# Kernel optimization log

Hardware: AMD Instinct MI355X
Metric: run time of the kernel (lower is better)

Reference implementation:

```python
import jax, jax.numpy as jnp
import numpy as np

NU, NP, H = 100000, 200000, 128
EV, EL = 500000, 150000


def _sage(x_src, x_dst, src, dst, Wl, bl, Wr, n_dst):
    # PyG SAGEConv: lin_l(mean_j x_j) + lin_r(x_i); lin_l has bias, lin_r does not.
    msg = x_src[src]                                             # [E, H] gather
    agg = jax.ops.segment_sum(msg, dst, num_segments=n_dst)      # [n_dst, H]
    cnt = jax.ops.segment_sum(jnp.ones((src.shape[0],), x_src.dtype), dst,
                              num_segments=n_dst)                # [n_dst]
    mean = agg / jnp.maximum(cnt, 1.0)[:, None]
    return mean @ Wl.T + bl + x_dst @ Wr.T


def _hetero_layer(xu, xp, Wl, bl, Wr, ev_s, ev_d, el_s, el_d):
    # relation order: 0 viewed(u->p), 1 rev_viewed(p->u), 2 liked(u->p), 3 rev_liked(p->u)
    post = (_sage(xu, xp, ev_s, ev_d, Wl[0], bl[0], Wr[0], NP)
            + _sage(xu, xp, el_s, el_d, Wl[2], bl[2], Wr[2], NP))
    user = (_sage(xp, xu, ev_d, ev_s, Wl[1], bl[1], Wr[1], NU)
            + _sage(xp, xu, el_d, el_s, Wl[3], bl[3], Wr[3], NU))
    return user, post


def setup_inputs() -> dict:
    key = jax.random.key(0)
    ks = jax.random.split(key, 9)
    s = 1.0 / np.sqrt(H)
    return {
        "emb_user": jax.random.normal(ks[0], (NU, H), jnp.float32),
        "emb_post": jax.random.normal(ks[1], (NP, H), jnp.float32),
        "W_l": jax.random.normal(ks[2], (2, 4, H, H), jnp.float32) * s,
        "b_l": jnp.zeros((2, 4, H), jnp.float32),
        "W_r": jax.random.normal(ks[3], (2, 4, H, H), jnp.float32) * s,
        "viewed_src": jax.random.randint(ks[4], (EV,), 0, NU, jnp.int32),
        "viewed_dst": jax.random.randint(ks[5], (EV,), 0, NP, jnp.int32),
        "liked_src": jax.random.randint(ks[6], (EL,), 0, NU, jnp.int32),
        "liked_dst": jax.random.randint(ks[7], (EL,), 0, NP, jnp.int32),
    }


def reference(emb_user, emb_post, W_l, b_l, W_r,
              viewed_src, viewed_dst, liked_src, liked_dst):
    xu, xp = _hetero_layer(emb_user, emb_post, W_l[0], b_l[0], W_r[0],
                           viewed_src, viewed_dst, liked_src, liked_dst)
    xu, xp = jax.nn.relu(xu), jax.nn.relu(xp)
    xu, xp = _hetero_layer(xu, xp, W_l[1], b_l[1], W_r[1],
                           viewed_src, viewed_dst, liked_src, liked_dst)
    return xu, xp
```

## Files before the change

kernel.cpp:

```cpp
#include <hip/hip_runtime.h>
#include <hip/hip_bf16.h>

#define H 128
#define IDX_CAP 2048

using bf16x8  = __attribute__((ext_vector_type(8))) short;
using floatx4 = __attribute__((ext_vector_type(4))) float;

static __device__ __forceinline__ short f2bf(float f) {
  union { float f; unsigned u; } v; v.f = f;
  unsigned r = v.u + 0x7fffu + ((v.u >> 16) & 1u);
  return (short)(r >> 16);
}
static __device__ __forceinline__ float bf2f(short s) {
  union { unsigned u; float f; } v; v.u = ((unsigned)(unsigned short)s) << 16;
  return v.f;
}

__global__ void count_edges(const int* __restrict__ src, const int* __restrict__ dst,
                            int E, int* __restrict__ cnt_s, int* __restrict__ cnt_d) {
  int e = blockIdx.x * blockDim.x + threadIdx.x;
  if (e >= E) return;
  atomicAdd(&cnt_s[src[e]], 1);
  atomicAdd(&cnt_d[dst[e]], 1);
}

__global__ __launch_bounds__(256) void scan_k1(const int* __restrict__ cnt, int* __restrict__ off,
                                               int* __restrict__ bsums, int4 starts, int4 lens) {
  int a = blockIdx.y;
  int start = ((const int*)&starts)[a];
  int len   = ((const int*)&lens)[a];
  int chunk = blockIdx.x * 1024;
  if (chunk >= len) return;
  const int* in = cnt + start;
  int* out = off + start;
  int tid = threadIdx.x;
  int base = chunk + tid * 4;
  int v[4];
#pragma unroll
  for (int j = 0; j < 4; ++j) v[j] = (base + j < len) ? in[base + j] : 0;
  int s = v[0] + v[1] + v[2] + v[3];
  __shared__ int lds[256];
  lds[tid] = s; __syncthreads();
  for (int o = 1; o < 256; o <<= 1) {
    int t = (tid >= o) ? lds[tid - o] : 0;
    __syncthreads();
    lds[tid] += t;
    __syncthreads();
  }
  int run = lds[tid] - s;
#pragma unroll
  for (int j = 0; j < 4; ++j) { if (base + j < len) out[base + j] = run; run += v[j]; }
  if (tid == 255) bsums[a * 256 + blockIdx.x] = lds[255];
}

__global__ __launch_bounds__(256) void scan_k2(int* __restrict__ bsums, int4 lens) {
  int a = blockIdx.x;
  int len = ((const int*)&lens)[a];
  int nb = (len + 1023) >> 10;
  int tid = threadIdx.x;
  int s = (tid < nb) ? bsums[a * 256 + tid] : 0;
  __shared__ int lds[256];
  lds[tid] = s; __syncthreads();
  for (int o = 1; o < 256; o <<= 1) {
    int t = (tid >= o) ? lds[tid - o] : 0;
    __syncthreads();
    lds[tid] += t;
    __syncthreads();
  }
  bsums[a * 256 + tid] = lds[tid] - s;
}

__global__ __launch_bounds__(256) void scan_k3(int* __restrict__ off, const int* __restrict__ bsums,
                                               int4 starts, int4 lens) {
  int a = blockIdx.y;
  int start = ((const int*)&starts)[a];
  int len   = ((const int*)&lens)[a];
  int chunk = blockIdx.x * 1024;
  if (chunk >= len) return;
  int add = bsums[a * 256 + blockIdx.x];
  int* out = off + start;
  int base = chunk + threadIdx.x * 4;
#pragma unroll
  for (int j = 0; j < 4; ++j) if (base + j < len) out[base + j] += add;
}

__global__ void fill_csr(const int* __restrict__ src, const int* __restrict__ dst, int E,
                         const int* __restrict__ off_d, int* __restrict__ cur_d, int* __restrict__ sort_d,
                         const int* __restrict__ off_s, int* __restrict__ cur_s, int* __restrict__ sort_s) {
  int e = blockIdx.x * blockDim.x + threadIdx.x;
  if (e >= E) return;
  int s = src[e], d = dst[e];
  sort_d[off_d[d] + atomicAdd(&cur_d[d], 1)] = s;
  sort_s[off_s[s] + atomicAdd(&cur_s[s], 1)] = d;
}

__global__ void cvt_bf16(const float* __restrict__ in, short* __restrict__ out, int n) {
  int idx = (blockIdx.x * blockDim.x + threadIdx.x) * 4;
  if (idx >= n) return;
  float4 v = *(const float4*)(in + idx);
  short4 o = { f2bf(v.x), f2bf(v.y), f2bf(v.z), f2bf(v.w) };
  *(short4*)(out + idx) = o;
}

static __device__ __forceinline__ int wswz(int e) {
  int n = e >> 7, k = e & 127;
  int jt = n >> 4, r = n & 15;
  int kk = k >> 5, q = (k >> 3) & 3, j = k & 7;
  return (((jt * 4 + kk) * 64 + q * 16 + r) << 3) + j;
}
__global__ void prep_weights(const float* __restrict__ W_l, const float* __restrict__ b_l,
                             const float* __restrict__ W_r,
                             short* __restrict__ Wbf, float* __restrict__ bc) {
  int i = blockIdx.x * blockDim.x + threadIdx.x;
  if (i >= 4 * 16384) return;
  int s = i >> 14, e = i & 16383;
  int l = s >> 1, t = s & 1;
  int rA = t ? 1 : 0, rB = t ? 3 : 2;
  const float* WA = W_l + ((size_t)(l * 4 + rA) << 14);
  const float* WB = W_l + ((size_t)(l * 4 + rB) << 14);
  const float* RA = W_r + ((size_t)(l * 4 + rA) << 14);
  const float* RB = W_r + ((size_t)(l * 4 + rB) << 14);
  short* o = Wbf + (size_t)s * 3 * 16384;
  int d = wswz(e);
  o[d]             = f2bf(WA[e]);
  o[16384 + d]     = f2bf(WB[e]);
  o[2 * 16384 + d] = f2bf(RA[e] + RB[e]);
  if (e < H) bc[s * H + e] = b_l[(l * 4 + rA) * H + e] + b_l[(l * 4 + rB) * H + e];
}

__global__ __launch_bounds__(512, 2) void fused_layer(
    const short* __restrict__ xgA, const short* __restrict__ xbA,
    const int* __restrict__ sVA, const int* __restrict__ oVA, const int* __restrict__ cVA,
    const int* __restrict__ sLA, const int* __restrict__ oLA, const int* __restrict__ cLA,
    const short* __restrict__ WAp, const float* __restrict__ biasA,
    float* __restrict__ o32A, short* __restrict__ o16A, int NA, int nbA,
    const short* __restrict__ xgB, const short* __restrict__ xbB,
    const int* __restrict__ sVB, const int* __restrict__ oVB, const int* __restrict__ cVB,
    const int* __restrict__ sLB, const int* __restrict__ oLB, const int* __restrict__ cLB,
    const short* __restrict__ WBp, const float* __restrict__ biasB,
    float* __restrict__ o32B, short* __restrict__ o16B, int NB, int relu) {
  extern __shared__ short smem[];
  short* Wlds = smem;
  int* idxLds = (int*)(smem + 3 * 16384);

  int b = blockIdx.x;
  const short *xg, *xb, *W; const int *sV, *oV, *cV, *sL, *oL, *cL;
  const float* bias; float* out32; short* out16; int N, nbPart, bLoc;
  if (b < nbA) {
    xg = xgA; xb = xbA; sV = sVA; oV = oVA; cV = cVA; sL = sLA; oL = oLA; cL = cLA;
    W = WAp; bias = biasA; out32 = o32A; out16 = o16A; N = NA; nbPart = nbA; bLoc = b;
  } else {
    xg = xgB; xb = xbB; sV = sVB; oV = oVB; cV = cVB; sL = sLB; oL = oLB; cL = cLB;
    W = WBp; bias = biasB; out32 = o32B; out16 = o16B; N = NB;
    nbPart = gridDim.x - nbA; bLoc = b - nbA;
  }

  int tid = threadIdx.x;
#pragma unroll
  for (int it = 0; it < 12; ++it) {
    int c = it * 512 + tid;
    *(bf16x8*)(Wlds + (size_t)c * 8) = *(const bf16x8*)(W + (size_t)c * 8);
  }
  __syncthreads();

  int wave = tid >> 6, lane = tid & 63;
  int r = lane & 15, quad = lane >> 4;
  int* myIdx = idxLds + wave * IDX_CAP;

  float bias_r[8];
#pragma unroll
  for (int jt = 0; jt < 8; ++jt) bias_r[jt] = bias[jt * 16 + r];

  int nrgTot = (N + 31) >> 5;
  int wStride = nbPart * 8;
  int wBase = bLoc * 8 + wave;

  floatx4 acc[2][8];

  for (int rg = wBase; rg < nrgTot; rg += wStride) {
    int rowb = rg << 5;

    bf16x8 afX[2][4];
#pragma unroll
    for (int t = 0; t < 2; ++t) {
      int row = rowb + t * 16 + r;
      row = row < N ? row : N - 1;
      const short* Xr = xb + (size_t)row * H + quad * 8;
#pragma unroll
      for (int kk = 0; kk < 4; ++kk) afX[t][kk] = *(const bf16x8*)(Xr + kk * 32);
    }

    int rbL = rowb + 31; rbL = rbL < N ? rbL : N - 1;
    int OV0 = oV[rowb];
    int lenV = oV[rbL] + cV[rbL] - OV0;
    int OL0 = oL[rowb];
    int lenL = oL[rbL] + cL[rbL] - OL0;
    int capV = lenV < IDX_CAP ? lenV : IDX_CAP;
    int rem = IDX_CAP - capV;
    int capL = lenL < rem ? lenL : rem;
    for (int k = lane; k < capV; k += 64) myIdx[k] = sV[OV0 + k];
    for (int k = lane; k < capL; k += 64) myIdx[capV + k] = sL[OL0 + k];

#pragma unroll
    for (int t = 0; t < 2; ++t)
#pragma unroll
      for (int j = 0; j < 8; ++j) acc[t][j] = floatx4{0.f, 0.f, 0.f, 0.f};

    bf16x8 afm[2][4];

    auto gatherRel = [&](const int* __restrict__ offA, const int* __restrict__ cntA,
                         const int* __restrict__ sG, int O0, int base, int cap) {
#pragma unroll
      for (int t = 0; t < 2; ++t) {
        int row = rowb + t * 16 + r;
        int node = row < N ? row : N - 1;
        int o = offA[node], n = cntA[node];
        int lo = o - O0;
        float ag[4][8];
#pragma unroll
        for (int kk = 0; kk < 4; ++kk)
#pragma unroll
          for (int j = 0; j < 8; ++j) ag[kk][j] = 0.f;

        auto gidx = [&](int i) -> int {
          int li = lo + i;
          return (li < cap) ? myIdx[base + li] : sG[o + i];
        };

        bf16x8 pA[4], pB[4];
        if (n > 0) {
          const short* xr = xg + (size_t)gidx(0) * H + quad * 8;
#pragma unroll
          for (int kk = 0; kk < 4; ++kk) pA[kk] = *(const bf16x8*)(xr + kk * 32);
        }
        if (n > 1) {
          const short* xr = xg + (size_t)gidx(1) * H + quad * 8;
#pragma unroll
          for (int kk = 0; kk < 4; ++kk) pB[kk] = *(const bf16x8*)(xr + kk * 32);
        }
        for (int i = 0; i < n; i += 2) {
          bf16x8 nA[4], nB[4];
          if (i + 2 < n) {
            const short* xr = xg + (size_t)gidx(i + 2) * H + quad * 8;
#pragma unroll
            for (int kk = 0; kk < 4; ++kk) nA[kk] = *(const bf16x8*)(xr + kk * 32);
          }
          if (i + 3 < n) {
            const short* xr = xg + (size_t)gidx(i + 3) * H + quad * 8;
#pragma unroll
            for (int kk = 0; kk < 4; ++kk) nB[kk] = *(const bf16x8*)(xr + kk * 32);
          }
#pragma unroll
          for (int kk = 0; kk < 4; ++kk)
#pragma unroll
            for (int j = 0; j < 8; ++j) ag[kk][j] += bf2f(pA[kk][j]);
          if (i + 1 < n) {
#pragma unroll
            for (int kk = 0; kk < 4; ++kk)
#pragma unroll
              for (int j = 0; j < 8; ++j) ag[kk][j] += bf2f(pB[kk][j]);
          }
#pragma unroll
          for (int kk = 0; kk < 4; ++kk) { pA[kk] = nA[kk]; pB[kk] = nB[kk]; }
        }
        float rin = 1.0f / fmaxf((float)n, 1.0f);
#pragma unroll
        for (int kk = 0; kk < 4; ++kk) {
          bf16x8 w;
#pragma unroll
          for (int j = 0; j < 8; ++j) w[j] = f2bf(ag[kk][j] * rin);
          afm[t][kk] = w;
        }
      }
    };

    auto mfmaMat = [&](int m, bf16x8 (&af)[2][4]) {
      const short* Wm = Wlds + m * 16384;
#pragma unroll
      for (int kk = 0; kk < 4; ++kk) {
#pragma unroll
        for (int jt = 0; jt < 8; ++jt) {
          bf16x8 bfR = *(const bf16x8*)(Wm + (size_t)((jt * 4 + kk) * 64 + lane) * 8);
          acc[0][jt] = __builtin_amdgcn_mfma_f32_16x16x32_bf16(af[0][kk], bfR, acc[0][jt], 0, 0, 0);
          acc[1][jt] = __builtin_amdgcn_mfma_f32_16x16x32_bf16(af[1][kk], bfR, acc[1][jt], 0, 0, 0);
        }
      }
    };

    gatherRel(oV, cV, sV, OV0, 0, capV);
    mfmaMat(0, afm);
    gatherRel(oL, cL, sL, OL0, capV, capL);
    mfmaMat(1, afm);
    mfmaMat(2, afX);

#pragma unroll
    for (int t = 0; t < 2; ++t) {
#pragma unroll
      for (int jt = 0; jt < 8; ++jt) {
        int ocol = jt * 16 + r;
        float bv = bias_r[jt];
#pragma unroll
        for (int g = 0; g < 4; ++g) {
          int orow = rowb + t * 16 + quad * 4 + g;
          if (orow < N) {
            float v = acc[t][jt][g] + bv;
            if (relu) v = fmaxf(v, 0.f);
            if (out32) out32[(size_t)orow * H + ocol] = v;
            else       out16[(size_t)orow * H + ocol] = f2bf(v);
          }
        }
      }
    }
  }
}

extern "C" void kernel_launch(void* const* d_in, const int* in_sizes, int n_in,
                              void* d_out, int out_size, void* d_ws, size_t ws_size,
                              hipStream_t stream) {
  const float* emb_user = (const float*)d_in[0];
  const float* emb_post = (const float*)d_in[1];
  const float* W_l = (const float*)d_in[2];
  const float* b_l = (const float*)d_in[3];
  const float* W_r = (const float*)d_in[4];
  const int* ev_s = (const int*)d_in[5];
  const int* ev_d = (const int*)d_in[6];
  const int* el_s = (const int*)d_in[7];
  const int* el_d = (const int*)d_in[8];

  const int NU = in_sizes[0] / H;
  const int NP = in_sizes[1] / H;
  const int EV = in_sizes[5];
  const int EL = in_sizes[7];
  const int T = 2 * NP + 2 * NU;
  const size_t NUH = (size_t)NU * H, NPH = (size_t)NP * H;

  char* p = (char*)d_ws;
  auto alloc = [&](size_t bytes) -> void* {
    void* q = (void*)p; p += (bytes + 255) & ~(size_t)255; return q;
  };
  int*   cnt   = (int*)alloc((size_t)T * 4);
  int*   cur   = (int*)alloc((size_t)T * 4);
  int*   off   = (int*)alloc((size_t)T * 4);
  int*   bsums = (int*)alloc(4 * 256 * 4);
  int*   sV_p  = (int*)alloc((size_t)EV * 4);
  int*   sV_u  = (int*)alloc((size_t)EV * 4);
  int*   sL_p  = (int*)alloc((size_t)EL * 4);
  int*   sL_u  = (int*)alloc((size_t)EL * 4);
  short* Wbf   = (short*)alloc((size_t)4 * 3 * 16384 * 2);
  float* bc    = (float*)alloc(4 * H * 4);
  short* xbf_u  = (short*)alloc(NUH * 2);
  short* xbf_p  = (short*)alloc(NPH * 2);
  short* xbf1_u = (short*)alloc(NUH * 2);
  short* xbf1_p = (short*)alloc(NPH * 2);

  float* out_u_final = (float*)d_out;
  float* out_p_final = (float*)d_out + NUH;

  const int oV_p = 0, oL_p = NP, oV_u = 2 * NP, oL_u = 2 * NP + NU;

  hipMemsetAsync(cnt, 0, (size_t)T * 4, stream);
  hipMemsetAsync(cur, 0, (size_t)T * 4, stream);
  count_edges<<<(EV + 255) / 256, 256, 0, stream>>>(ev_s, ev_d, EV, cnt + oV_u, cnt + oV_p);
  count_edges<<<(EL + 255) / 256, 256, 0, stream>>>(el_s, el_d, EL, cnt + oL_u, cnt + oL_p);

  int4 starts = { oV_p, oL_p, oV_u, oL_u };
  int4 lens   = { NP, NP, NU, NU };
  int maxb = ((NP > NU ? NP : NU) + 1023) / 1024;
  dim3 gscan(maxb, 4, 1);
  scan_k1<<<gscan, 256, 0, stream>>>(cnt, off, bsums, starts, lens);
  scan_k2<<<4, 256, 0, stream>>>(bsums, lens);
  scan_k3<<<gscan, 256, 0, stream>>>(off, bsums, starts, lens);

  fill_csr<<<(EV + 255) / 256, 256, 0, stream>>>(ev_s, ev_d, EV,
                                                 off + oV_p, cur + oV_p, sV_p,
                                                 off + oV_u, cur + oV_u, sV_u);
  fill_csr<<<(EL + 255) / 256, 256, 0, stream>>>(el_s, el_d, EL,
                                                 off + oL_p, cur + oL_p, sL_p,
                                                 off + oL_u, cur + oL_u, sL_u);

  cvt_bf16<<<((int)(NUH / 4) + 255) / 256, 256, 0, stream>>>(emb_user, xbf_u, (int)NUH);
  cvt_bf16<<<((int)(NPH / 4) + 255) / 256, 256, 0, stream>>>(emb_post, xbf_p, (int)NPH);
  prep_weights<<<(4 * 16384 + 255) / 256, 256, 0, stream>>>(W_l, b_l, W_r, Wbf, bc);

  hipFuncSetAttribute((const void*)fused_layer, hipFuncAttributeMaxDynamicSharedMemorySize,
                      160 * 1024);

  long long wP = (long long)(EV + EL) + 3LL * NP;
  long long wU = (long long)(EV + EL) + 3LL * NU;
  int nbP = (int)((256LL * wP) / (wP + wU));
  if (nbP < 1) nbP = 1;
  if (nbP > 255) nbP = 255;

  for (int l = 0; l < 2; ++l) {
    const short* xu = l ? xbf1_u : xbf_u;
    const short* xp = l ? xbf1_p : xbf_p;
    const short* Wpost = Wbf + (size_t)(l * 2 + 0) * 3 * 16384;
    const short* Wuser = Wbf + (size_t)(l * 2 + 1) * 3 * 16384;
    const float* bpost = bc + (l * 2 + 0) * H;
    const float* buser = bc + (l * 2 + 1) * H;

    fused_layer<<<256, 512, 160 * 1024, stream>>>(
        xu, xp, sV_p, off + oV_p, cnt + oV_p, sL_p, off + oL_p, cnt + oL_p,
        Wpost, bpost, l ? out_p_final : nullptr, l ? nullptr : xbf1_p, NP, nbP,
        xp, xu, sV_u, off + oV_u, cnt + oV_u, sL_u, off + oL_u, cnt + oL_u,
        Wuser, buser, l ? out_u_final : nullptr, l ? nullptr : xbf1_u, NU, l == 0);
  }
}
```

Before: 810.3 us.

## Shrink fused_layer LDS, read root weights from global, merge preprocessing kernels

Shared memory in fused_layer is cut: only the two neighbor-weight matrices stay in LDS, the combined root weight is read straight from global (cache), and the per-wave index buffer drops from 2048 to 384 entries. Launch bounds are raised to 4 blocks of 512 threads to allow more resident waves. The paired count_edges, fill_csr and cvt_bf16 launches are each merged into one kernel to cut launch overhead. The tighter register budget can cause spills in the MFMA accumulator loop. The grid stays at 256 blocks, so extra occupancy may never be used, while global weight reads add latency.

```diff
diff --git a/kernel.cpp b/kernel.cpp
--- a/kernel.cpp
+++ b/kernel.cpp
@@ -2,7 +2,7 @@
 #include <hip/hip_bf16.h>
 
 #define H 128
-#define IDX_CAP 2048
+#define IDX_CAP 384
 
 using bf16x8  = __attribute__((ext_vector_type(8))) short;
 using floatx4 = __attribute__((ext_vector_type(4))) float;
@@ -17,12 +17,18 @@
   return v.f;
 }
 
-__global__ void count_edges(const int* __restrict__ src, const int* __restrict__ dst,
-                            int E, int* __restrict__ cnt_s, int* __restrict__ cnt_d) {
-  int e = blockIdx.x * blockDim.x + threadIdx.x;
-  if (e >= E) return;
-  atomicAdd(&cnt_s[src[e]], 1);
-  atomicAdd(&cnt_d[dst[e]], 1);
+__global__ void count_edges2(const int* __restrict__ ev_s, const int* __restrict__ ev_d, int EV,
+                             const int* __restrict__ el_s, const int* __restrict__ el_d, int EL,
+                             int* __restrict__ cnt, int oV_u, int oV_p, int oL_u, int oL_p) {
+  int i = blockIdx.x * blockDim.x + threadIdx.x;
+  if (i < EV) {
+    atomicAdd(&cnt[oV_u + ev_s[i]], 1);
+    atomicAdd(&cnt[oV_p + ev_d[i]], 1);
+  } else if (i - EV < EL) {
+    int e = i - EV;
+    atomicAdd(&cnt[oL_u + el_s[e]], 1);
+    atomicAdd(&cnt[oL_p + el_d[e]], 1);
+  }
 }
 
 __global__ __launch_bounds__(256) void scan_k1(const int* __restrict__ cnt, int* __restrict__ off,
@@ -85,22 +91,38 @@
   for (int j = 0; j < 4; ++j) if (base + j < len) out[base + j] += add;
 }
 
-__global__ void fill_csr(const int* __restrict__ src, const int* __restrict__ dst, int E,
-                         const int* __restrict__ off_d, int* __restrict__ cur_d, int* __restrict__ sort_d,
-                         const int* __restrict__ off_s, int* __restrict__ cur_s, int* __restrict__ sort_s) {
-  int e = blockIdx.x * blockDim.x + threadIdx.x;
-  if (e >= E) return;
-  int s = src[e], d = dst[e];
-  sort_d[off_d[d] + atomicAdd(&cur_d[d], 1)] = s;
-  sort_s[off_s[s] + atomicAdd(&cur_s[s], 1)] = d;
-}
-
-__global__ void cvt_bf16(const float* __restrict__ in, short* __restrict__ out, int n) {
+__global__ void fill_csr2(const int* __restrict__ ev_s, const int* __restrict__ ev_d, int EV,
+                          const int* __restrict__ el_s, const int* __restrict__ el_d, int EL,
+                          const int* __restrict__ off, int* __restrict__ cur,
+                          int* __restrict__ sV_p, int* __restrict__ sV_u,
+                          int* __restrict__ sL_p, int* __restrict__ sL_u,
+                          int oV_p, int oV_u, int oL_p, int oL_u) {
+  int i = blockIdx.x * blockDim.x + threadIdx.x;
+  if (i < EV) {
+    int s = ev_s[i], d = ev_d[i];
+    sV_p[off[oV_p + d] + atomicAdd(&cur[oV_p + d], 1)] = s;
+    sV_u[off[oV_u + s] + atomicAdd(&cur[oV_u + s], 1)] = d;
+  } else if (i - EV < EL) {
+    int e = i - EV;
+    int s = el_s[e], d = el_d[e];
+    sL_p[off[oL_p + d] + atomicAdd(&cur[oL_p + d], 1)] = s;
+    sL_u[off[oL_u + s] + atomicAdd(&cur[oL_u + s], 1)] = d;
+  }
+}
+
+__global__ void cvt_bf16_2(const float* __restrict__ inU, short* __restrict__ outU, int nU,
+                           const float* __restrict__ inP, short* __restrict__ outP, int nP) {
   int idx = (blockIdx.x * blockDim.x + threadIdx.x) * 4;
-  if (idx >= n) return;
-  float4 v = *(const float4*)(in + idx);
+  const float* in; short* out;
+  if (idx < nU) { in = inU + idx; out = outU + idx; }
+  else {
+    idx -= nU;
+    if (idx >= nP) return;
+    in = inP + idx; out = outP + idx;
+  }
+  float4 v = *(const float4*)in;
   short4 o = { f2bf(v.x), f2bf(v.y), f2bf(v.z), f2bf(v.w) };
-  *(short4*)(out + idx) = o;
+  *(short4*)out = o;
 }
 
 static __device__ __forceinline__ int wswz(int e) {
@@ -129,7 +151,7 @@
   if (e < H) bc[s * H + e] = b_l[(l * 4 + rA) * H + e] + b_l[(l * 4 + rB) * H + e];
 }
 
-__global__ __launch_bounds__(512, 2) void fused_layer(
+__global__ __launch_bounds__(512, 4) void fused_layer(
     const short* __restrict__ xgA, const short* __restrict__ xbA,
     const int* __restrict__ sVA, const int* __restrict__ oVA, const int* __restrict__ cVA,
     const int* __restrict__ sLA, const int* __restrict__ oLA, const int* __restrict__ cLA,
@@ -142,7 +164,7 @@
     float* __restrict__ o32B, short* __restrict__ o16B, int NB, int relu) {
   extern __shared__ short smem[];
   short* Wlds = smem;
-  int* idxLds = (int*)(smem + 3 * 16384);
+  int* idxLds = (int*)(smem + 2 * 16384);
 
   int b = blockIdx.x;
   const short *xg, *xb, *W; const int *sV, *oV, *cV, *sL, *oL, *cL;
@@ -158,7 +180,7 @@
 
   int tid = threadIdx.x;
 #pragma unroll
-  for (int it = 0; it < 12; ++it) {
+  for (int it = 0; it < 8; ++it) {
     int c = it * 512 + tid;
     *(bf16x8*)(Wlds + (size_t)c * 8) = *(const bf16x8*)(W + (size_t)c * 8);
   }
@@ -275,7 +297,7 @@
       }
     };
 
-    auto mfmaMat = [&](int m, bf16x8 (&af)[2][4]) {
+    auto mfmaLds = [&](int m, bf16x8 (&af)[2][4]) {
       const short* Wm = Wlds + m * 16384;
 #pragma unroll
       for (int kk = 0; kk < 4; ++kk) {
@@ -288,11 +310,24 @@
       }
     };
 
+    auto mfmaGlb = [&](bf16x8 (&af)[2][4]) {
+      const short* Wm = W + 2 * 16384;
+#pragma unroll
+      for (int kk = 0; kk < 4; ++kk) {
+#pragma unroll
+        for (int jt = 0; jt < 8; ++jt) {
+          bf16x8 bfR = *(const bf16x8*)(Wm + (size_t)((jt * 4 + kk) * 64 + lane) * 8);
+          acc[0][jt] = __builtin_amdgcn_mfma_f32_16x16x32_bf16(af[0][kk], bfR, acc[0][jt], 0, 0, 0);
+          acc[1][jt] = __builtin_amdgcn_mfma_f32_16x16x32_bf16(af[1][kk], bfR, acc[1][jt], 0, 0, 0);
+        }
+      }
+    };
+
     gatherRel(oV, cV, sV, OV0, 0, capV);
-    mfmaMat(0, afm);
+    mfmaLds(0, afm);
     gatherRel(oL, cL, sL, OL0, capV, capL);
-    mfmaMat(1, afm);
-    mfmaMat(2, afX);
+    mfmaLds(1, afm);
+    mfmaGlb(afX);
 
 #pragma unroll
     for (int t = 0; t < 2; ++t) {
@@ -361,8 +396,8 @@
 
   hipMemsetAsync(cnt, 0, (size_t)T * 4, stream);
   hipMemsetAsync(cur, 0, (size_t)T * 4, stream);
-  count_edges<<<(EV + 255) / 256, 256, 0, stream>>>(ev_s, ev_d, EV, cnt + oV_u, cnt + oV_p);
-  count_edges<<<(EL + 255) / 256, 256, 0, stream>>>(el_s, el_d, EL, cnt + oL_u, cnt + oL_p);
+  count_edges2<<<(EV + EL + 255) / 256, 256, 0, stream>>>(
+      ev_s, ev_d, EV, el_s, el_d, EL, cnt, oV_u, oV_p, oL_u, oL_p);
 
   int4 starts = { oV_p, oL_p, oV_u, oL_u };
   int4 lens   = { NP, NP, NU, NU };
@@ -372,19 +407,17 @@
   scan_k2<<<4, 256, 0, stream>>>(bsums, lens);
   scan_k3<<<gscan, 256, 0, stream>>>(off, bsums, starts, lens);
 
-  fill_csr<<<(EV + 255) / 256, 256, 0, stream>>>(ev_s, ev_d, EV,
-                                                 off + oV_p, cur + oV_p, sV_p,
-                                                 off + oV_u, cur + oV_u, sV_u);
-  fill_csr<<<(EL + 255) / 256, 256, 0, stream>>>(el_s, el_d, EL,
-                                                 off + oL_p, cur + oL_p, sL_p,
-                                                 off + oL_u, cur + oL_u, sL_u);
-
-  cvt_bf16<<<((int)(NUH / 4) + 255) / 256, 256, 0, stream>>>(emb_user, xbf_u, (int)NUH);
-  cvt_bf16<<<((int)(NPH / 4) + 255) / 256, 256, 0, stream>>>(emb_post, xbf_p, (int)NPH);
+  fill_csr2<<<(EV + EL + 255) / 256, 256, 0, stream>>>(
+      ev_s, ev_d, EV, el_s, el_d, EL, off, cur,
+      sV_p, sV_u, sL_p, sL_u, oV_p, oV_u, oL_p, oL_u);
+
+  cvt_bf16_2<<<((int)((NUH + NPH) / 4) + 255) / 256, 256, 0, stream>>>(
+      emb_user, xbf_u, (int)NUH, emb_post, xbf_p, (int)NPH);
   prep_weights<<<(4 * 16384 + 255) / 256, 256, 0, stream>>>(W_l, b_l, W_r, Wbf, bc);
 
+  const int ldsBytes = 2 * 16384 * 2 + 8 * IDX_CAP * 4;
   hipFuncSetAttribute((const void*)fused_layer, hipFuncAttributeMaxDynamicSharedMemorySize,
-                      160 * 1024);
+                      ldsBytes);
 
   long long wP = (long long)(EV + EL) + 3LL * NP;
   long long wU = (long long)(EV + EL) + 3LL * NU;
@@ -400,7 +433,7 @@
     const float* bpost = bc + (l * 2 + 0) * H;
     const float* buser = bc + (l * 2 + 1) * H;
 
-    fused_layer<<<256, 512, 160 * 1024, stream>>>(
+    fused_layer<<<256, 512, ldsBytes, stream>>>(
         xu, xp, sV_p, off + oV_p, cnt + oV_p, sL_p, off + oL_p, cnt + oL_p,
         Wpost, bpost, l ? out_p_final : nullptr, l ? nullptr : xbf1_p, NP, nbP,
         xp, xu, sV_u, off + oV_u, cnt + oV_u, sL_u, off + oL_u, cnt + oL_u,
```

Measured after the change: 1.609 ms. 1.99x slower.
